# Kernel tuning notes

Hardware: AMD Instinct MI355X
Metric: run time of the kernel (lower is better)

The kernel has to match this reference:

```python
import jax, jax.numpy as jnp
import numpy as np

POOL_SIZE = 4
MAX_DIM = 256
GRID = MAX_DIM // POOL_SIZE  # 64
NUM_CELLS = GRID * GRID      # 4096
B = 64                        # static max_batch (batch.max()+1 in torch)
N = 1_000_000
C = 64


def setup_inputs() -> dict:
    key = jax.random.key(0)
    k1, k2, k3 = jax.random.split(key, 3)
    x = jax.random.normal(k1, (N, C), dtype=jnp.float32)
    pos = jax.random.randint(k2, (N, 2), 0, MAX_DIM, dtype=jnp.int64)
    batch = jnp.sort(jax.random.randint(k3, (N,), 0, B, dtype=jnp.int64))
    return {"x": x, "pos": pos, "batch": batch}


def reference(x, pos, batch):
    # voxel key: (batch, pos_x//pool, pos_y//pool) -> flat cell index
    qpos = pos[:, :2] // POOL_SIZE                       # [N, 2] int
    idx = batch * NUM_CELLS + qpos[:, 0] * GRID + qpos[:, 1]  # [N]
    num_seg = B * NUM_CELLS
    # scatter_reduce(amax, include_self=False): max over points in each cell
    pooled = jax.ops.segment_max(x, idx, num_segments=num_seg)  # empty -> -inf
    # cells with no points stay zero (output_x initialized to zeros in torch)
    counts = jax.ops.segment_sum(jnp.ones((x.shape[0], 1), x.dtype), idx,
                                 num_segments=num_seg)          # [num_seg, 1]
    pooled = jnp.where(counts > 0, pooled, jnp.zeros((), x.dtype))
    # [B, grid^2, C] -> flatten -> [B, grid^2 * C]
    return pooled.reshape(B, NUM_CELLS * x.shape[1])
```

## Files before the change

### kernel.cpp

```cpp
#include <hip/hip_runtime.h>

#define POOL_SHIFT 2
#define GRID_DIM 64
#define NUM_CELLS 4096
#define NCH 64
#define BATCH 64
#define QCS 16
#define SENTINEL ((int)0x80000000)

typedef float vf4 __attribute__((ext_vector_type(4)));

__global__ __launch_bounds__(256) void bounds_kernel(
    const int* __restrict__ batch, int* __restrict__ bstart, int n) {
    int p = blockIdx.x * blockDim.x + threadIdx.x;
    if (p >= n) return;
    int b = batch[p];
    if (p == 0) {
        for (int i = 0; i <= b; ++i) bstart[i] = 0;
    } else {
        int pb = batch[p - 1];
        for (int i = pb + 1; i <= b; ++i) bstart[i] = p;
    }
    if (p == n - 1) {
        for (int i = b + 1; i <= BATCH; ++i) bstart[i] = n;
    }
}

__device__ __forceinline__ int fmap(float f) {
    int i = __float_as_int(f);
    return i >= 0 ? i : (i ^ 0x7fffffff);
}
__device__ __forceinline__ float funmap(int m) {
    if (m == SENTINEL) return 0.0f;
    return __int_as_float(m >= 0 ? m : (m ^ 0x7fffffff));
}

__device__ __forceinline__ void accum(int* acc, int2 pp, vf4 v) {
    int c = ((pp.x >> POOL_SHIFT) << 6) | (pp.y >> POOL_SHIFT);
    atomicMax(&acc[0 * NUM_CELLS + c], fmap(v.x));
    atomicMax(&acc[1 * NUM_CELLS + c], fmap(v.y));
    atomicMax(&acc[2 * NUM_CELLS + c], fmap(v.z));
    atomicMax(&acc[3 * NUM_CELLS + c], fmap(v.w));
}

__global__ __launch_bounds__(256, 2) void pool_kernel(
    const float* __restrict__ x, const int* __restrict__ pos,
    const int* __restrict__ bstart, float* __restrict__ out) {
    __shared__ int acc[4 * NUM_CELLS];
    const int L  = (int)blockIdx.x;
    const int b  = ((L >> 7) << 3) | (L & 7);
    const int qc = (L >> 3) & 15;
    const int t  = threadIdx.x;

    for (int i = t; i < 4 * NUM_CELLS; i += 256) acc[i] = SENTINEL;
    __syncthreads();

    const int r0 = bstart[b], r1 = bstart[b + 1];
    const vf4* xq  = (const vf4*)x;
    const int2* pq = (const int2*)pos;

    int r = r0 + t;
    for (; r + 768 < r1; r += 1024) {
        int2 pp0 = pq[r];
        int2 pp1 = pq[r + 256];
        int2 pp2 = pq[r + 512];
        int2 pp3 = pq[r + 768];
        vf4 v0 = xq[(size_t)r * QCS + qc];
        vf4 v1 = xq[(size_t)(r + 256) * QCS + qc];
        vf4 v2 = xq[(size_t)(r + 512) * QCS + qc];
        vf4 v3 = xq[(size_t)(r + 768) * QCS + qc];
        accum(acc, pp0, v0);
        accum(acc, pp1, v1);
        accum(acc, pp2, v2);
        accum(acc, pp3, v3);
    }
    for (; r < r1; r += 256) {
        int2 pp = pq[r];
        vf4 v = xq[(size_t)r * QCS + qc];
        accum(acc, pp, v);
    }
    __syncthreads();

    const size_t obase = (size_t)b * NUM_CELLS * NCH + (size_t)qc * 4;
    for (int c = t; c < NUM_CELLS; c += 256) {
        vf4 o;
        o.x = funmap(acc[0 * NUM_CELLS + c]);
        o.y = funmap(acc[1 * NUM_CELLS + c]);
        o.z = funmap(acc[2 * NUM_CELLS + c]);
        o.w = funmap(acc[3 * NUM_CELLS + c]);
        *(vf4*)&out[obase + (size_t)c * NCH] = o;
    }
}

extern "C" void kernel_launch(void* const* d_in, const int* in_sizes, int n_in,
                              void* d_out, int out_size, void* d_ws, size_t ws_size,
                              hipStream_t stream) {
    const float* x   = (const float*)d_in[0];
    const int* pos   = (const int*)d_in[1];
    const int* batch = (const int*)d_in[2];
    float* out = (float*)d_out;
    int n = in_sizes[2];

    int* bstart = (int*)d_ws;

    bounds_kernel<<<(n + 255) / 256, 256, 0, stream>>>(batch, bstart, n);
    pool_kernel<<<BATCH * QCS, 256, 0, stream>>>(x, pos, bstart, out);
}
```

Before: 408.9 us.

## Widen channel slice per block to 8 and use 1024-thread blocks with swizzled LDS

Each block now handles 8 channels instead of 4, using a 128KB dynamic LDS accumulator and 1024 threads. This halves the number of blocks that reread the pos array per batch, and each point reads 32 contiguous bytes of x. Per-channel XOR swizzling of the cell index is meant to spread atomics from one point across LDS banks. The cost is fewer blocks (512), a large LDS footprint that limits residency to about one block per CU, and a changed block-to-batch ordering.

```diff
diff --git a/kernel.cpp b/kernel.cpp
--- a/kernel.cpp
+++ b/kernel.cpp
@@ -5,7 +5,7 @@
 #define NUM_CELLS 4096
 #define NCH 64
 #define BATCH 64
-#define QCS 16
+#define OCS 8
 #define SENTINEL ((int)0x80000000)
 
 typedef float vf4 __attribute__((ext_vector_type(4)));
@@ -35,60 +35,75 @@
     return __int_as_float(m >= 0 ? m : (m ^ 0x7fffffff));
 }
 
-__device__ __forceinline__ void accum(int* acc, int2 pp, vf4 v) {
+__device__ __forceinline__ void accum8(int* acc, int2 pp, vf4 a, vf4 b2) {
     int c = ((pp.x >> POOL_SHIFT) << 6) | (pp.y >> POOL_SHIFT);
-    atomicMax(&acc[0 * NUM_CELLS + c], fmap(v.x));
-    atomicMax(&acc[1 * NUM_CELLS + c], fmap(v.y));
-    atomicMax(&acc[2 * NUM_CELLS + c], fmap(v.z));
-    atomicMax(&acc[3 * NUM_CELLS + c], fmap(v.w));
+    atomicMax(&acc[0 * NUM_CELLS + (c ^ 0)],  fmap(a.x));
+    atomicMax(&acc[1 * NUM_CELLS + (c ^ 4)],  fmap(a.y));
+    atomicMax(&acc[2 * NUM_CELLS + (c ^ 8)],  fmap(a.z));
+    atomicMax(&acc[3 * NUM_CELLS + (c ^ 12)], fmap(a.w));
+    atomicMax(&acc[4 * NUM_CELLS + (c ^ 16)], fmap(b2.x));
+    atomicMax(&acc[5 * NUM_CELLS + (c ^ 20)], fmap(b2.y));
+    atomicMax(&acc[6 * NUM_CELLS + (c ^ 24)], fmap(b2.z));
+    atomicMax(&acc[7 * NUM_CELLS + (c ^ 28)], fmap(b2.w));
 }
 
-__global__ __launch_bounds__(256, 2) void pool_kernel(
+__global__ __launch_bounds__(1024, 4) void pool_kernel(
     const float* __restrict__ x, const int* __restrict__ pos,
     const int* __restrict__ bstart, float* __restrict__ out) {
-    __shared__ int acc[4 * NUM_CELLS];
+    extern __shared__ int acc[];
     const int L  = (int)blockIdx.x;
-    const int b  = ((L >> 7) << 3) | (L & 7);
-    const int qc = (L >> 3) & 15;
+    const int b  = L & 63;
+    const int oc = L >> 6;
     const int t  = threadIdx.x;
 
-    for (int i = t; i < 4 * NUM_CELLS; i += 256) acc[i] = SENTINEL;
+    for (int i = t; i < 8 * NUM_CELLS; i += 1024) acc[i] = SENTINEL;
     __syncthreads();
 
     const int r0 = bstart[b], r1 = bstart[b + 1];
     const vf4* xq  = (const vf4*)x;
     const int2* pq = (const int2*)pos;
+    const int q0 = oc * 2;
 
     int r = r0 + t;
-    for (; r + 768 < r1; r += 1024) {
+    for (; r + 3072 < r1; r += 4096) {
         int2 pp0 = pq[r];
-        int2 pp1 = pq[r + 256];
-        int2 pp2 = pq[r + 512];
-        int2 pp3 = pq[r + 768];
-        vf4 v0 = xq[(size_t)r * QCS + qc];
-        vf4 v1 = xq[(size_t)(r + 256) * QCS + qc];
-        vf4 v2 = xq[(size_t)(r + 512) * QCS + qc];
-        vf4 v3 = xq[(size_t)(r + 768) * QCS + qc];
-        accum(acc, pp0, v0);
-        accum(acc, pp1, v1);
-        accum(acc, pp2, v2);
-        accum(acc, pp3, v3);
+        int2 pp1 = pq[r + 1024];
+        int2 pp2 = pq[r + 2048];
+        int2 pp3 = pq[r + 3072];
+        vf4 a0 = xq[(size_t)r * 16 + q0];
+        vf4 b0 = xq[(size_t)r * 16 + q0 + 1];
+        vf4 a1 = xq[(size_t)(r + 1024) * 16 + q0];
+        vf4 b1 = xq[(size_t)(r + 1024) * 16 + q0 + 1];
+        vf4 a2 = xq[(size_t)(r + 2048) * 16 + q0];
+        vf4 b2 = xq[(size_t)(r + 2048) * 16 + q0 + 1];
+        vf4 a3 = xq[(size_t)(r + 3072) * 16 + q0];
+        vf4 b3 = xq[(size_t)(r + 3072) * 16 + q0 + 1];
+        accum8(acc, pp0, a0, b0);
+        accum8(acc, pp1, a1, b1);
+        accum8(acc, pp2, a2, b2);
+        accum8(acc, pp3, a3, b3);
     }
-    for (; r < r1; r += 256) {
+    for (; r < r1; r += 1024) {
         int2 pp = pq[r];
-        vf4 v = xq[(size_t)r * QCS + qc];
-        accum(acc, pp, v);
+        vf4 a = xq[(size_t)r * 16 + q0];
+        vf4 b2 = xq[(size_t)r * 16 + q0 + 1];
+        accum8(acc, pp, a, b2);
     }
     __syncthreads();
 
-    const size_t obase = (size_t)b * NUM_CELLS * NCH + (size_t)qc * 4;
-    for (int c = t; c < NUM_CELLS; c += 256) {
-        vf4 o;
-        o.x = funmap(acc[0 * NUM_CELLS + c]);
-        o.y = funmap(acc[1 * NUM_CELLS + c]);
-        o.z = funmap(acc[2 * NUM_CELLS + c]);
-        o.w = funmap(acc[3 * NUM_CELLS + c]);
-        *(vf4*)&out[obase + (size_t)c * NCH] = o;
+    const size_t obase = (size_t)b * NUM_CELLS * NCH + (size_t)oc * 8;
+    for (int c = t; c < NUM_CELLS; c += 1024) {
+        vf4 o0, o1;
+        o0.x = funmap(acc[0 * NUM_CELLS + (c ^ 0)]);
+        o0.y = funmap(acc[1 * NUM_CELLS + (c ^ 4)]);
+        o0.z = funmap(acc[2 * NUM_CELLS + (c ^ 8)]);
+        o0.w = funmap(acc[3 * NUM_CELLS + (c ^ 12)]);
+        o1.x = funmap(acc[4 * NUM_CELLS + (c ^ 16)]);
+        o1.y = funmap(acc[5 * NUM_CELLS + (c ^ 20)]);
+        o1.z = funmap(acc[6 * NUM_CELLS + (c ^ 24)]);
+        o1.w = funmap(acc[7 * NUM_CELLS + (c ^ 28)]);
+        *(vf4*)&out[obase + (size_t)c * NCH]     = o0;
+        *(vf4*)&out[obase + (size_t)c * NCH + 4] = o1;
     }
 }
 
@@ -104,5 +119,6 @@
     int* bstart = (int*)d_ws;
 
     bounds_kernel<<<(n + 255) / 256, 256, 0, stream>>>(batch, bstart, n);
-    pool_kernel<<<BATCH * QCS, 256, 0, stream>>>(x, pos, bstart, out);
+    pool_kernel<<<BATCH * OCS, 1024, 8 * NUM_CELLS * sizeof(int), stream>>>(
+        x, pos, bstart, out);
 }
```

Result: no change. 416.8 us (+1.9%).
